# Optimization experiments

Hardware: AMD Instinct MI355X
Metric: run time of the kernel (lower is better)

## Reference

```python
import jax, jax.numpy as jnp
import numpy as np

DIM = 96
K = 3
STRIDE = 1
PAD = 1
RED = 4
BN_EPS = 1e-5


def setup_inputs() -> dict:
    key = jax.random.key(0)
    ks = jax.random.split(key, 8)
    b, c, h, w = 32, DIM, 128, 128
    cr = DIM // RED
    return {
        "x": jax.random.normal(ks[0], (b, c, h, w), jnp.float32),
        "w1": jax.random.normal(ks[1], (cr, c), jnp.float32) * 0.1,          # conv1 1x1, no bias
        "gamma": jnp.ones((cr,), jnp.float32),
        "beta": jnp.zeros((cr,), jnp.float32),
        "running_mean": jax.random.normal(ks[2], (cr,), jnp.float32) * 0.1,
        "running_var": jax.random.uniform(ks[3], (cr,), jnp.float32, 0.5, 1.5),
        "w2": jax.random.normal(ks[4], (DIM * K * K, cr), jnp.float32) * 0.1,  # conv2 1x1
        "b2": jax.random.normal(ks[5], (DIM * K * K,), jnp.float32) * 0.1,
        "bias": jnp.zeros((DIM,), jnp.float32),
    }


def _dynamic_weight(x, w1, gamma, beta, running_mean, running_var, w2, b2):
    # AdaptiveAvgPool2d((1,1)) -> [b, c]
    pooled = jnp.mean(x, axis=(2, 3))
    # conv1 (1x1, no bias) on 1x1 spatial == matmul
    h1 = pooled @ w1.T  # [b, c//r]
    # BatchNorm2d in inference mode (running stats)
    h1 = (h1 - running_mean) * jax.lax.rsqrt(running_var + BN_EPS) * gamma + beta
    h1 = jax.nn.sigmoid(h1)
    # conv2 (1x1) == matmul + bias -> [b, dim*k*k]
    wdyn = h1 @ w2.T + b2
    return wdyn.reshape(x.shape[0], DIM, K, K)


def _per_sample_depthwise(x, weight, bias):
    # x: [b, c, h, w], weight: [b, c, k, k] -> per-sample depthwise conv
    def one(xi, wi):
        # xi: [c,h,w], wi: [c,k,k]
        out = jax.lax.conv_general_dilated(
            xi[None], wi[:, None],
            window_strides=(STRIDE, STRIDE),
            padding=[(PAD, PAD), (PAD, PAD)],
            dimension_numbers=("NCHW", "OIHW", "NCHW"),
            feature_group_count=DIM,
        )
        return out[0]

    y = jax.vmap(one)(x, weight)  # [b, c, h', w']
    return y + bias[None, :, None, None]


def reference(x, w1, gamma, beta, running_mean, running_var, w2, b2, bias):
    weight = _dynamic_weight(x, w1, gamma, beta, running_mean, running_var, w2, b2)
    return _per_sample_depthwise(x, weight, bias)
```

## Files before the change

### kernel.cpp

```cpp
#include <hip/hip_runtime.h>
#include <math.h>

#define C_DIM 96
#define CR 24
#define H_DIM 128
#define W_DIM 128
#define B_DIM 32

__global__ void pool_kernel(const float* __restrict__ x, float* __restrict__ pooled) {
    int plane = blockIdx.x;
    const float4* xp = (const float4*)(x + (size_t)plane * (H_DIM * W_DIM));
    float s = 0.f;
    for (int i = threadIdx.x; i < 4096; i += 256) {
        float4 v = xp[i];
        s += v.x + v.y + v.z + v.w;
    }
    for (int off = 32; off; off >>= 1) s += __shfl_down(s, off, 64);
    __shared__ float ls[4];
    int lane = threadIdx.x & 63, wv = threadIdx.x >> 6;
    if (lane == 0) ls[wv] = s;
    __syncthreads();
    if (threadIdx.x == 0) {
        float t = ls[0] + ls[1] + ls[2] + ls[3];
        pooled[plane] = t * (1.f / (H_DIM * W_DIM));
    }
}

__global__ void wdyn_kernel(const float* __restrict__ pooled,
                            const float* __restrict__ w1,
                            const float* __restrict__ gamma,
                            const float* __restrict__ beta,
                            const float* __restrict__ rmean,
                            const float* __restrict__ rvar,
                            const float* __restrict__ w2,
                            const float* __restrict__ b2,
                            float* __restrict__ wdyn) {
    int b = blockIdx.x;
    int tid = threadIdx.x;
    __shared__ float pl[C_DIM];
    __shared__ float h1[CR];
    if (tid < C_DIM) pl[tid] = pooled[b * C_DIM + tid];
    __syncthreads();
    if (tid < CR) {
        float s = 0.f;
        const float* wr = w1 + tid * C_DIM;
        for (int c = 0; c < C_DIM; c++) s += pl[c] * wr[c];
        s = (s - rmean[tid]) * rsqrtf(rvar[tid] + 1e-5f) * gamma[tid] + beta[tid];
        h1[tid] = 1.f / (1.f + expf(-s));
    }
    __syncthreads();
    for (int o = tid; o < C_DIM * 9; o += 256) {
        float s = b2[o];
        const float* wr = w2 + o * CR;
        #pragma unroll
        for (int j = 0; j < CR; j++) s += h1[j] * wr[j];
        wdyn[b * (C_DIM * 9) + o] = s;
    }
}

__global__ void __launch_bounds__(256) dwconv_kernel(const float* __restrict__ x,
                                                     const float* __restrict__ wdyn,
                                                     const float* __restrict__ bias,
                                                     float* __restrict__ out) {
    int gid = blockIdx.x * 256 + threadIdx.x;
    int col = gid & (W_DIM - 1);
    int plane = gid >> 7;
    int c = plane % C_DIM;
    const float* xp = x + (size_t)plane * (H_DIM * W_DIM);
    float* op = out + (size_t)plane * (H_DIM * W_DIM);
    const float* wp = wdyn + (size_t)plane * 9;
    float w00 = wp[0], w01 = wp[1], w02 = wp[2];
    float w10 = wp[3], w11 = wp[4], w12 = wp[5];
    float w20 = wp[6], w21 = wp[7], w22 = wp[8];
    float bb = bias[c];
    const bool hasL = (col > 0), hasR = (col < W_DIM - 1);

    float p0 = 0.f, p1 = 0.f, p2 = 0.f;
    float c0, c1, c2, n0, n1, n2;
    c0 = hasL ? xp[col - 1] : 0.f;
    c1 = xp[col];
    c2 = hasR ? xp[col + 1] : 0.f;

    #pragma unroll 4
    for (int r = 0; r < H_DIM; r++) {
        if (r < H_DIM - 1) {
            const float* row = xp + (r + 1) * W_DIM;
            n0 = hasL ? row[col - 1] : 0.f;
            n1 = row[col];
            n2 = hasR ? row[col + 1] : 0.f;
        } else {
            n0 = n1 = n2 = 0.f;
        }
        float s = w00 * p0 + w01 * p1 + w02 * p2
                + w10 * c0 + w11 * c1 + w12 * c2
                + w20 * n0 + w21 * n1 + w22 * n2 + bb;
        op[r * W_DIM + col] = s;
        p0 = c0; p1 = c1; p2 = c2;
        c0 = n0; c1 = n1; c2 = n2;
    }
}

extern "C" void kernel_launch(void* const* d_in, const int* in_sizes, int n_in,
                              void* d_out, int out_size, void* d_ws, size_t ws_size,
                              hipStream_t stream) {
    const float* x     = (const float*)d_in[0];
    const float* w1    = (const float*)d_in[1];
    const float* gamma = (const float*)d_in[2];
    const float* beta  = (const float*)d_in[3];
    const float* rmean = (const float*)d_in[4];
    const float* rvar  = (const float*)d_in[5];
    const float* w2    = (const float*)d_in[6];
    const float* b2    = (const float*)d_in[7];
    const float* bias  = (const float*)d_in[8];
    float* out = (float*)d_out;

    float* pooled = (float*)d_ws;
    float* wdyn   = pooled + B_DIM * C_DIM;

    pool_kernel<<<B_DIM * C_DIM, 256, 0, stream>>>(x, pooled);
    wdyn_kernel<<<B_DIM, 256, 0, stream>>>(pooled, w1, gamma, beta, rmean, rvar, w2, b2, wdyn);
    int total_threads = B_DIM * C_DIM * W_DIM;
    dwconv_kernel<<<total_threads / 256, 256, 0, stream>>>(x, wdyn, bias, out);
}
```

Measured before the change: 426.0 us.

## Vectorize depthwise conv to float4 columns with shuffle halos and row chunks

The depthwise conv kernel now has each thread own four adjacent columns, loaded as float4, and take the left and right halo values from neighbouring lanes with wavefront shuffles instead of extra scalar loads. Each plane's rows are split into four chunks so the thread count stays the same and parallelism is kept. This reduces load and store instruction count and redundant halo reads. The cost is one extra halo row read per chunk. The shuffles rely on 32-lane groups lining up inside the 64-wide wavefront.

```diff
diff --git a/kernel.cpp b/kernel.cpp
--- a/kernel.cpp
+++ b/kernel.cpp
@@ -6,6 +6,8 @@
 #define H_DIM 128
 #define W_DIM 128
 #define B_DIM 32
+#define CHUNKS 4
+#define ROWS_PER_CHUNK (H_DIM / CHUNKS)
 
 __global__ void pool_kernel(const float* __restrict__ x, float* __restrict__ pooled) {
     int plane = blockIdx.x;
@@ -62,10 +64,14 @@
                                                      const float* __restrict__ wdyn,
                                                      const float* __restrict__ bias,
                                                      float* __restrict__ out) {
-    int gid = blockIdx.x * 256 + threadIdx.x;
-    int col = gid & (W_DIM - 1);
-    int plane = gid >> 7;
+    int T = blockIdx.x * 256 + threadIdx.x;
+    int g = T & 31;
+    int chunk = (T >> 5) & 3;
+    int plane = T >> 7;
     int c = plane % C_DIM;
+    int col = g << 2;
+    int r0 = chunk * ROWS_PER_CHUNK;
+
     const float* xp = x + (size_t)plane * (H_DIM * W_DIM);
     float* op = out + (size_t)plane * (H_DIM * W_DIM);
     const float* wp = wdyn + (size_t)plane * 9;
@@ -73,30 +79,54 @@
     float w10 = wp[3], w11 = wp[4], w12 = wp[5];
     float w20 = wp[6], w21 = wp[7], w22 = wp[8];
     float bb = bias[c];
-    const bool hasL = (col > 0), hasR = (col < W_DIM - 1);
+    const bool leftEdge = (g == 0), rightEdge = (g == 31);
 
-    float p0 = 0.f, p1 = 0.f, p2 = 0.f;
-    float c0, c1, c2, n0, n1, n2;
-    c0 = hasL ? xp[col - 1] : 0.f;
-    c1 = xp[col];
-    c2 = hasR ? xp[col + 1] : 0.f;
+    float4 pv, cv, nv;
+    float pl, pr, cl, cr_, nl, nr;
+
+    {
+        int r = r0 - 1;
+        float4 v;
+        if (r >= 0) v = *(const float4*)(xp + r * W_DIM + col);
+        else { v.x = v.y = v.z = v.w = 0.f; }
+        float l = __shfl_up(v.w, 1, 64);
+        float rr = __shfl_down(v.x, 1, 64);
+        pv = v; pl = leftEdge ? 0.f : l; pr = rightEdge ? 0.f : rr;
+    }
+    {
+        float4 v = *(const float4*)(xp + r0 * W_DIM + col);
+        float l = __shfl_up(v.w, 1, 64);
+        float rr = __shfl_down(v.x, 1, 64);
+        cv = v; cl = leftEdge ? 0.f : l; cr_ = rightEdge ? 0.f : rr;
+    }
 
     #pragma unroll 4
-    for (int r = 0; r < H_DIM; r++) {
-        if (r < H_DIM - 1) {
-            const float* row = xp + (r + 1) * W_DIM;
-            n0 = hasL ? row[col - 1] : 0.f;
-            n1 = row[col];
-            n2 = hasR ? row[col + 1] : 0.f;
-        } else {
-            n0 = n1 = n2 = 0.f;
-        }
-        float s = w00 * p0 + w01 * p1 + w02 * p2
-                + w10 * c0 + w11 * c1 + w12 * c2
-                + w20 * n0 + w21 * n1 + w22 * n2 + bb;
-        op[r * W_DIM + col] = s;
-        p0 = c0; p1 = c1; p2 = c2;
-        c0 = n0; c1 = n1; c2 = n2;
+    for (int i = 0; i < ROWS_PER_CHUNK; i++) {
+        int r = r0 + i;
+        float4 v;
+        if (r + 1 < H_DIM) v = *(const float4*)(xp + (r + 1) * W_DIM + col);
+        else { v.x = v.y = v.z = v.w = 0.f; }
+        float l = __shfl_up(v.w, 1, 64);
+        float rr = __shfl_down(v.x, 1, 64);
+        nv = v; nl = leftEdge ? 0.f : l; nr = rightEdge ? 0.f : rr;
+
+        float4 o;
+        o.x = w00 * pl   + w01 * pv.x + w02 * pv.y
+            + w10 * cl   + w11 * cv.x + w12 * cv.y
+            + w20 * nl   + w21 * nv.x + w22 * nv.y + bb;
+        o.y = w00 * pv.x + w01 * pv.y + w02 * pv.z
+            + w10 * cv.x + w11 * cv.y + w12 * cv.z
+            + w20 * nv.x + w21 * nv.y + w22 * nv.z + bb;
+        o.z = w00 * pv.y + w01 * pv.z + w02 * pv.w
+            + w10 * cv.y + w11 * cv.z + w12 * cv.w
+            + w20 * nv.y + w21 * nv.z + w22 * nv.w + bb;
+        o.w = w00 * pv.z + w01 * pv.w + w02 * pr
+            + w10 * cv.z + w11 * cv.w + w12 * cr_
+            + w20 * nv.z + w21 * nv.w + w22 * nr + bb;
+        *(float4*)(op + r * W_DIM + col) = o;
+
+        pv = cv; pl = cl; pr = cr_;
+        cv = nv; cl = nl; cr_ = nr;
     }
 }
 
@@ -119,6 +149,6 @@
 
     pool_kernel<<<B_DIM * C_DIM, 256, 0, stream>>>(x, pooled);
     wdyn_kernel<<<B_DIM, 256, 0, stream>>>(pooled, w1, gamma, beta, rmean, rvar, w2, b2, wdyn);
-    int total_threads = B_DIM * C_DIM * W_DIM;
+    int total_threads = B_DIM * C_DIM * CHUNKS * (W_DIM / 4);
     dwconv_kernel<<<total_threads / 256, 256, 0, stream>>>(x, wdyn, bias, out);
 }
```

After: 396.1 us. 1.08x faster.
